# Performance work log

Measured on AMD Instinct MI355X. Metric: run time of the kernel, lower is better.

## Reference

```python
import jax, jax.numpy as jnp
import numpy as np

N_NODES = 100000


def gcn_conv(x, src, dst, W, b):
    # torch_geometric GCNConv: add self-loops, sym-normalize, linear, aggregate
    n = x.shape[0]
    deg = jax.ops.segment_sum(jnp.ones_like(src, dtype=x.dtype), dst, num_segments=n)
    dinv = jnp.where(deg > 0, jax.lax.rsqrt(deg), 0.0)
    norm = dinv[src] * dinv[dst]                      # [E]
    h = x @ W                                         # [N, out]
    msg = h[src] * norm[:, None]                      # [E, out] gather
    out = jax.ops.segment_sum(msg, dst, num_segments=n)  # scatter-add
    return out + b


def add_self_loops(edge_index, n):
    loop = jnp.arange(n, dtype=edge_index.dtype)
    src = jnp.concatenate([edge_index[0], loop])
    dst = jnp.concatenate([edge_index[1], loop])
    return src, dst


def setup_inputs() -> dict:
    key = jax.random.key(0)
    k1, k2, k3, k4 = jax.random.split(key, 4)
    F_in, F_mid = 64, 32
    x = jax.random.normal(k1, (N_NODES, F_in), dtype=jnp.float32)
    edge_index = jax.random.randint(k2, (2, 1200000), 0, N_NODES, dtype=jnp.int64)
    W1 = jax.random.normal(k3, (F_in, F_mid), dtype=jnp.float32) * (1.0 / np.sqrt(F_in))
    b1 = jnp.zeros((F_mid,), dtype=jnp.float32)
    W2 = jax.random.normal(k4, (F_mid, F_in), dtype=jnp.float32) * (1.0 / np.sqrt(F_mid))
    b2 = jnp.zeros((F_in,), dtype=jnp.float32)
    return {"x": x, "edge_index": edge_index, "W1": W1, "b1": b1, "W2": W2, "b2": b2}


def reference(x, edge_index, W1, b1, W2, b2):
    src, dst = add_self_loops(edge_index, x.shape[0])
    h = jax.nn.relu(gcn_conv(x, src, dst, W1, b1))
    # F.dropout in eval mode is identity (module not in training)
    out = gcn_conv(h, src, dst, W2, b2)
    return out
```

## Files before the change

kernel.cpp:

```cpp
#include <hip/hip_runtime.h>


#define CAP 32
#define OVF_MAX 65536
#define SH_BITS 8
#define SH 256
#define BCAP 3584
#define EPB 4096
#define EPT 16

__device__ __forceinline__ unsigned bf16rn(float f) {
    unsigned u = __float_as_uint(f);
    return (u + 0x7fffu + ((u >> 16) & 1u)) >> 16;
}
__device__ __forceinline__ unsigned pack2(float f0, float f1) {
    return (bf16rn(f1) << 16) | bf16rn(f0);
}
__device__ __forceinline__ void acc2(float4& a, uint2 v) {
    a.x += __uint_as_float(v.x << 16);
    a.y += __uint_as_float(v.x & 0xffff0000u);
    a.z += __uint_as_float(v.y << 16);
    a.w += __uint_as_float(v.y & 0xffff0000u);
}

__global__ void init_kernel(int* __restrict__ bcur, int* __restrict__ ovfcnt,
                            unsigned int* __restrict__ g1rowN,
                            unsigned int* __restrict__ q1rowN, int B) {
    int i = blockIdx.x * blockDim.x + threadIdx.x;
    if (i < B) bcur[i] = i * BCAP;
    if (i == 0) *ovfcnt = 0;
    if (i < 16) { g1rowN[i] = 0u; q1rowN[i] = 0u; }
}

__global__ __launch_bounds__(256) void bin_kernel(const int* __restrict__ src,
                                                  const int* __restrict__ dst,
                                                  int* __restrict__ bcur,
                                                  unsigned int* __restrict__ ebuf,
                                                  int* __restrict__ ovfcnt,
                                                  int* __restrict__ ovf, int E, int B) {
    __shared__ int h[512];
    __shared__ int gp[512];
    __shared__ int lr[512];
    for (int b = threadIdx.x; b < B; b += 256) { h[b] = 0; lr[b] = 0; }
    __syncthreads();
    int base = blockIdx.x * EPB;
    int s[EPT], d[EPT], bk[EPT];
#pragma unroll
    for (int k = 0; k < EPT; ++k) {
        int e = base + k * 256 + threadIdx.x;
        bool ok = e < E;
        s[k]  = ok ? src[e] : 0;
        d[k]  = ok ? dst[e] : 0;
        bk[k] = ok ? (d[k] >> SH_BITS) : -1;
        if (ok) atomicAdd(&h[bk[k]], 1);
    }
    __syncthreads();
    for (int b = threadIdx.x; b < B; b += 256)
        if (h[b]) gp[b] = atomicAdd(&bcur[b], h[b]);
    __syncthreads();
#pragma unroll
    for (int k = 0; k < EPT; ++k) {
        if (bk[k] >= 0) {
            int r = atomicAdd(&lr[bk[k]], 1);
            int pos = gp[bk[k]] + r;
            if (pos < (bk[k] + 1) * BCAP)
                ebuf[pos] = ((unsigned)(d[k] & (SH - 1)) << 24) | (unsigned)s[k];
            else { int o = atomicAdd(ovfcnt, 1); if (o < OVF_MAX) { ovf[2 * o] = s[k]; ovf[2 * o + 1] = d[k]; } }
        }
    }
}

__global__ __launch_bounds__(256) void fillb_kernel(const unsigned int* __restrict__ ebuf,
                                                    const int* __restrict__ bcur,
                                                    int* __restrict__ adj,
                                                    float* __restrict__ dinv,
                                                    int* __restrict__ ovfcnt,
                                                    int* __restrict__ ovf, int N) {
    __shared__ int lcnt[SH];
    __shared__ int ladj[SH * CAP];
    int b = blockIdx.x;
    for (int i = threadIdx.x; i < SH; i += 256) lcnt[i] = 0;
    for (int i = threadIdx.x; i < SH * CAP; i += 256) ladj[i] = N;
    __syncthreads();
    int beg = b * BCAP;
    int tot = bcur[b] - beg;
    int m = tot < BCAP ? tot : BCAP;
    for (int i = threadIdx.x; i < m; i += 256) {
        unsigned p = ebuf[beg + i];
        int ld = (int)(p >> 24), sidx = (int)(p & 0xFFFFFF);
        int q = atomicAdd(&lcnt[ld], 1);
        if (q < CAP) ladj[ld * CAP + q] = sidx;
        else { int o = atomicAdd(ovfcnt, 1); if (o < OVF_MAX) { ovf[2 * o] = sidx; ovf[2 * o + 1] = (b << SH_BITS) + ld; } }
    }
    __syncthreads();
    int nb0 = b << SH_BITS;
    const int4* l4 = (const int4*)ladj;
    int4* a4 = (int4*)(adj + (size_t)nb0 * CAP);
    for (int i = threadIdx.x; i < SH * CAP / 4; i += 256) {
        int nd = nb0 + (i * 4) / CAP;
        if (nd < N) a4[i] = l4[i];
    }
    for (int i = threadIdx.x; i < SH; i += 256) {
        int nd = nb0 + i;
        if (nd < N) dinv[nd] = rsqrtf((float)lcnt[i] + 1.0f);
    }
}

__global__ __launch_bounds__(256) void gemm1_kernel(const float* __restrict__ x,
                                                    const float* __restrict__ W1,
                                                    const float* __restrict__ dinv,
                                                    unsigned int* __restrict__ g1, int N) {
    __shared__ float Ws[64 * 32];
    __shared__ float xs[16][64];
    int tid = threadIdx.x;
    const float4* W4 = (const float4*)W1;
    float4* Ws4 = (float4*)Ws;
    for (int i = tid; i < 512; i += 256) Ws4[i] = W4[i];
    int nb = blockIdx.x * 16;
    {
        int ln = tid >> 4, k4 = (tid & 15) * 4;
        int n = nb + ln;
        float4 v = make_float4(0.f, 0.f, 0.f, 0.f);
        if (n < N) v = *(const float4*)(x + (size_t)n * 64 + k4);
        *(float4*)(&xs[ln][k4]) = v;
    }
    __syncthreads();
    int ln = tid >> 4, j = tid & 15;
    int n = nb + ln;
    if (n < N) {
        float s0 = 0.f, s1 = 0.f;
#pragma unroll
        for (int k = 0; k < 64; ++k) {
            float xv = xs[ln][k];
            s0 += xv * Ws[k * 32 + 2 * j];
            s1 += xv * Ws[k * 32 + 2 * j + 1];
        }
        float dv = dinv[n];
        g1[(size_t)n * 16 + j] = pack2(dv * s0, dv * s1);
    }
}

__device__ __forceinline__ float4 gather_row4(const int4* __restrict__ adj4,
                                              const int* __restrict__ ovfcnt,
                                              const int* __restrict__ ovf,
                                              const uint2* __restrict__ g2,
                                              int n, int l, int N) {
    int4 idx = adj4[(size_t)n * 8 + l];
    float4 a = make_float4(0.f, 0.f, 0.f, 0.f);
    uint2 self = g2[(size_t)n * 8 + l];
    {
        int s0  = __shfl(idx.x, 0, 8), s1  = __shfl(idx.y, 0, 8);
        int s2  = __shfl(idx.z, 0, 8), s3  = __shfl(idx.w, 0, 8);
        int s4  = __shfl(idx.x, 1, 8), s5  = __shfl(idx.y, 1, 8);
        int s6  = __shfl(idx.z, 1, 8), s7  = __shfl(idx.w, 1, 8);
        int s8  = __shfl(idx.x, 2, 8), s9  = __shfl(idx.y, 2, 8);
        int s10 = __shfl(idx.z, 2, 8), s11 = __shfl(idx.w, 2, 8);
        int s12 = __shfl(idx.x, 3, 8), s13 = __shfl(idx.y, 3, 8);
        int s14 = __shfl(idx.z, 3, 8), s15 = __shfl(idx.w, 3, 8);
        uint2 v0  = g2[(size_t)s0  * 8 + l], v1  = g2[(size_t)s1  * 8 + l];
        uint2 v2  = g2[(size_t)s2  * 8 + l], v3  = g2[(size_t)s3  * 8 + l];
        uint2 v4  = g2[(size_t)s4  * 8 + l], v5  = g2[(size_t)s5  * 8 + l];
        uint2 v6  = g2[(size_t)s6  * 8 + l], v7  = g2[(size_t)s7  * 8 + l];
        uint2 v8  = g2[(size_t)s8  * 8 + l], v9  = g2[(size_t)s9  * 8 + l];
        uint2 v10 = g2[(size_t)s10 * 8 + l], v11 = g2[(size_t)s11 * 8 + l];
        uint2 v12 = g2[(size_t)s12 * 8 + l], v13 = g2[(size_t)s13 * 8 + l];
        uint2 v14 = g2[(size_t)s14 * 8 + l], v15 = g2[(size_t)s15 * 8 + l];
        acc2(a, self);
        acc2(a, v0);  acc2(a, v1);  acc2(a, v2);  acc2(a, v3);
        acc2(a, v4);  acc2(a, v5);  acc2(a, v6);  acc2(a, v7);
        acc2(a, v8);  acc2(a, v9);  acc2(a, v10); acc2(a, v11);
        acc2(a, v12); acc2(a, v13); acc2(a, v14); acc2(a, v15);
    }
    if (__shfl(idx.x, 4, 8) != N) {
        int s0  = __shfl(idx.x, 4, 8), s1  = __shfl(idx.y, 4, 8);
        int s2  = __shfl(idx.z, 4, 8), s3  = __shfl(idx.w, 4, 8);
        int s4  = __shfl(idx.x, 5, 8), s5  = __shfl(idx.y, 5, 8);
        int s6  = __shfl(idx.z, 5, 8), s7  = __shfl(idx.w, 5, 8);
        int s8  = __shfl(idx.x, 6, 8), s9  = __shfl(idx.y, 6, 8);
        int s10 = __shfl(idx.z, 6, 8), s11 = __shfl(idx.w, 6, 8);
        int s12 = __shfl(idx.x, 7, 8), s13 = __shfl(idx.y, 7, 8);
        int s14 = __shfl(idx.z, 7, 8), s15 = __shfl(idx.w, 7, 8);
        uint2 v0  = g2[(size_t)s0  * 8 + l], v1  = g2[(size_t)s1  * 8 + l];
        uint2 v2  = g2[(size_t)s2  * 8 + l], v3  = g2[(size_t)s3  * 8 + l];
        uint2 v4  = g2[(size_t)s4  * 8 + l], v5  = g2[(size_t)s5  * 8 + l];
        uint2 v6  = g2[(size_t)s6  * 8 + l], v7  = g2[(size_t)s7  * 8 + l];
        uint2 v8  = g2[(size_t)s8  * 8 + l], v9  = g2[(size_t)s9  * 8 + l];
        uint2 v10 = g2[(size_t)s10 * 8 + l], v11 = g2[(size_t)s11 * 8 + l];
        uint2 v12 = g2[(size_t)s12 * 8 + l], v13 = g2[(size_t)s13 * 8 + l];
        uint2 v14 = g2[(size_t)s14 * 8 + l], v15 = g2[(size_t)s15 * 8 + l];
        acc2(a, v0);  acc2(a, v1);  acc2(a, v2);  acc2(a, v3);
        acc2(a, v4);  acc2(a, v5);  acc2(a, v6);  acc2(a, v7);
        acc2(a, v8);  acc2(a, v9);  acc2(a, v10); acc2(a, v11);
        acc2(a, v12); acc2(a, v13); acc2(a, v14); acc2(a, v15);
    }
    int c = *ovfcnt; if (c > OVF_MAX) c = OVF_MAX;
    for (int i = 0; i < c; ++i) {
        if (ovf[2 * i + 1] == n) acc2(a, g2[(size_t)ovf[2 * i] * 8 + l]);
    }
    return a;
}

__global__ void gather_q_kernel(const int4* __restrict__ adj4,
                                const int* __restrict__ ovfcnt, const int* __restrict__ ovf,
                                const uint2* __restrict__ g2, const float* __restrict__ dinv,
                                const float* __restrict__ b1, uint2* __restrict__ q2, int N) {
    int tid = blockIdx.x * blockDim.x + threadIdx.x;
    int n = tid >> 3, l = tid & 7;
    if (n < N) {
        float4 a = gather_row4(adj4, ovfcnt, ovf, g2, n, l, N);
        float dv = dinv[n];
        float4 bb = ((const float4*)b1)[l];
        float vx = dv * a.x + bb.x, vy = dv * a.y + bb.y;
        float vz = dv * a.z + bb.z, vw = dv * a.w + bb.w;
        vx = vx > 0.f ? vx : 0.f; vy = vy > 0.f ? vy : 0.f;
        vz = vz > 0.f ? vz : 0.f; vw = vw > 0.f ? vw : 0.f;
        q2[(size_t)n * 8 + l] = make_uint2(pack2(dv * vx, dv * vy), pack2(dv * vz, dv * vw));
    }
}

__global__ __launch_bounds__(256) void gather_out_kernel(
        const int4* __restrict__ adj4,
        const int* __restrict__ ovfcnt, const int* __restrict__ ovf,
        const uint2* __restrict__ q2, const float* __restrict__ dinv,
        const float* __restrict__ W2, const float* __restrict__ b2,
        float* __restrict__ out, int N) {
    __shared__ float Ws[32 * 64];
    __shared__ float sAgg[32][36];
    int tid = threadIdx.x;
    const float4* W4 = (const float4*)W2;
    float4* Ws4 = (float4*)Ws;
    for (int i = tid; i < 512; i += 256) Ws4[i] = W4[i];
    int nb = blockIdx.x * 32;
    int o = tid >> 3, l = tid & 7;
    int n = nb + o;
    if (n < N) *(float4*)(&sAgg[o][l * 4]) = gather_row4(adj4, ovfcnt, ovf, q2, n, l, N);
    __syncthreads();
    int ln = tid >> 6, j = tid & 63;
#pragma unroll
    for (int nn = 0; nn < 8; ++nn) {
        int ol = nn * 4 + ln;
        int node = nb + ol;
        if (node < N) {
            float s = 0.f;
#pragma unroll
            for (int k = 0; k < 32; ++k) s += sAgg[ol][k] * Ws[k * 64 + j];
            out[(size_t)node * 64 + j] = dinv[node] * s + b2[j];
        }
    }
}

extern "C" void kernel_launch(void* const* d_in, const int* in_sizes, int n_in,
                              void* d_out, int out_size, void* d_ws, size_t ws_size,
                              hipStream_t stream) {
    const float* x  = (const float*)d_in[0];
    const int*   ei = (const int*)d_in[1];
    const float* W1 = (const float*)d_in[2];
    const float* b1 = (const float*)d_in[3];
    const float* W2 = (const float*)d_in[4];
    const float* b2 = (const float*)d_in[5];
    float* out = (float*)d_out;

    int N = in_sizes[0] / 64;
    int E = in_sizes[1] / 2;
    const int* src = ei;
    const int* dst = ei + (size_t)E;
    int B = (N + SH - 1) >> SH_BITS;

    size_t NP = (size_t)N + 1;
    float* dinv   = (float*)d_ws;
    unsigned int* g1 = (unsigned int*)(dinv + N);
    unsigned int* q1 = g1 + 16 * NP;
    unsigned int* ebuf = q1;
    int*   adj    = (int*)(q1 + 16 * NP);
    int*   bcur   = adj + (size_t)CAP * N;
    int*   ovfcnt = bcur + 512;
    int*   ovf    = ovfcnt + 4;

    init_kernel<<<(B + 255) / 256, 256, 0, stream>>>(bcur, ovfcnt,
                                                     g1 + 16 * (size_t)N, q1 + 16 * (size_t)N, B);
    bin_kernel<<<(E + EPB - 1) / EPB, 256, 0, stream>>>(src, dst, bcur, ebuf, ovfcnt, ovf, E, B);
    fillb_kernel<<<B, 256, 0, stream>>>(ebuf, bcur, adj, dinv, ovfcnt, ovf, N);

    gemm1_kernel<<<(N + 15) / 16, 256, 0, stream>>>(x, W1, dinv, g1, N);

    long long tq = (long long)N * 8;
    gather_q_kernel<<<(int)((tq + 255) / 256), 256, 0, stream>>>(
        (const int4*)adj, ovfcnt, ovf, (const uint2*)g1, dinv, b1, (uint2*)q1, N);
    gather_out_kernel<<<(N + 31) / 32, 256, 0, stream>>>(
        (const int4*)adj, ovfcnt, ovf, (const uint2*)q1, dinv, W2, b2, out, N);
}
```

Before: 178.2 us.

## Skip unused adjacency halves, reuse bin-kernel atomic ranks, add nontemporal output stores

The adjacency list is now read in two 64-byte halves, and the second half is loaded only when the 16th slot of the first half is occupied. fillb writes the second half only for nodes with at least 16 neighbours. bin_kernel keeps the rank returned by the histogram atomic, which removes the second shared-memory counter and its atomics. The final output uses nontemporal stores. The aim is to cut adjacency memory traffic and atomics, at the cost of a dependent second load for high-degree nodes and relying on stale memory never being read.

```diff
diff --git a/kernel.cpp b/kernel.cpp
--- a/kernel.cpp
+++ b/kernel.cpp
@@ -40,19 +40,17 @@
                                                   int* __restrict__ ovf, int E, int B) {
     __shared__ int h[512];
     __shared__ int gp[512];
-    __shared__ int lr[512];
-    for (int b = threadIdx.x; b < B; b += 256) { h[b] = 0; lr[b] = 0; }
+    for (int b = threadIdx.x; b < B; b += 256) h[b] = 0;
     __syncthreads();
     int base = blockIdx.x * EPB;
-    int s[EPT], d[EPT], bk[EPT];
+    int s[EPT], d[EPT], r[EPT];
 #pragma unroll
     for (int k = 0; k < EPT; ++k) {
         int e = base + k * 256 + threadIdx.x;
         bool ok = e < E;
-        s[k]  = ok ? src[e] : 0;
-        d[k]  = ok ? dst[e] : 0;
-        bk[k] = ok ? (d[k] >> SH_BITS) : -1;
-        if (ok) atomicAdd(&h[bk[k]], 1);
+        s[k] = ok ? src[e] : 0;
+        d[k] = ok ? dst[e] : 0;
+        r[k] = ok ? atomicAdd(&h[d[k] >> SH_BITS], 1) : 0;
     }
     __syncthreads();
     for (int b = threadIdx.x; b < B; b += 256)
@@ -60,10 +58,11 @@
     __syncthreads();
 #pragma unroll
     for (int k = 0; k < EPT; ++k) {
-        if (bk[k] >= 0) {
-            int r = atomicAdd(&lr[bk[k]], 1);
-            int pos = gp[bk[k]] + r;
-            if (pos < (bk[k] + 1) * BCAP)
+        int e = base + k * 256 + threadIdx.x;
+        if (e < E) {
+            int bk = d[k] >> SH_BITS;
+            int pos = gp[bk] + r[k];
+            if (pos < (bk + 1) * BCAP)
                 ebuf[pos] = ((unsigned)(d[k] & (SH - 1)) << 24) | (unsigned)s[k];
             else { int o = atomicAdd(ovfcnt, 1); if (o < OVF_MAX) { ovf[2 * o] = s[k]; ovf[2 * o + 1] = d[k]; } }
         }
@@ -97,8 +96,10 @@
     const int4* l4 = (const int4*)ladj;
     int4* a4 = (int4*)(adj + (size_t)nb0 * CAP);
     for (int i = threadIdx.x; i < SH * CAP / 4; i += 256) {
-        int nd = nb0 + (i * 4) / CAP;
-        if (nd < N) a4[i] = l4[i];
+        int row = i >> 3;
+        int nd = nb0 + row;
+        bool second = (i & 4) != 0;
+        if (nd < N && (!second || lcnt[row] >= 16)) a4[i] = l4[i];
     }
     for (int i = threadIdx.x; i < SH; i += 256) {
         int nd = nb0 + i;
@@ -140,23 +141,24 @@
     }
 }
 
-__device__ __forceinline__ float4 gather_row4(const int4* __restrict__ adj4,
+__device__ __forceinline__ float4 gather_row4(const int2* __restrict__ adj2,
                                               const int* __restrict__ ovfcnt,
                                               const int* __restrict__ ovf,
                                               const uint2* __restrict__ g2,
                                               int n, int l, int N) {
-    int4 idx = adj4[(size_t)n * 8 + l];
+    int2 h1 = adj2[(size_t)n * 16 + l];
     float4 a = make_float4(0.f, 0.f, 0.f, 0.f);
     uint2 self = g2[(size_t)n * 8 + l];
+    int s15;
     {
-        int s0  = __shfl(idx.x, 0, 8), s1  = __shfl(idx.y, 0, 8);
-        int s2  = __shfl(idx.z, 0, 8), s3  = __shfl(idx.w, 0, 8);
-        int s4  = __shfl(idx.x, 1, 8), s5  = __shfl(idx.y, 1, 8);
-        int s6  = __shfl(idx.z, 1, 8), s7  = __shfl(idx.w, 1, 8);
-        int s8  = __shfl(idx.x, 2, 8), s9  = __shfl(idx.y, 2, 8);
-        int s10 = __shfl(idx.z, 2, 8), s11 = __shfl(idx.w, 2, 8);
-        int s12 = __shfl(idx.x, 3, 8), s13 = __shfl(idx.y, 3, 8);
-        int s14 = __shfl(idx.z, 3, 8), s15 = __shfl(idx.w, 3, 8);
+        int s0  = __shfl(h1.x, 0, 8), s1  = __shfl(h1.y, 0, 8);
+        int s2  = __shfl(h1.x, 1, 8), s3  = __shfl(h1.y, 1, 8);
+        int s4  = __shfl(h1.x, 2, 8), s5  = __shfl(h1.y, 2, 8);
+        int s6  = __shfl(h1.x, 3, 8), s7  = __shfl(h1.y, 3, 8);
+        int s8  = __shfl(h1.x, 4, 8), s9  = __shfl(h1.y, 4, 8);
+        int s10 = __shfl(h1.x, 5, 8), s11 = __shfl(h1.y, 5, 8);
+        int s12 = __shfl(h1.x, 6, 8), s13 = __shfl(h1.y, 6, 8);
+        int s14 = __shfl(h1.x, 7, 8); s15 = __shfl(h1.y, 7, 8);
         uint2 v0  = g2[(size_t)s0  * 8 + l], v1  = g2[(size_t)s1  * 8 + l];
         uint2 v2  = g2[(size_t)s2  * 8 + l], v3  = g2[(size_t)s3  * 8 + l];
         uint2 v4  = g2[(size_t)s4  * 8 + l], v5  = g2[(size_t)s5  * 8 + l];
@@ -171,15 +173,16 @@
         acc2(a, v8);  acc2(a, v9);  acc2(a, v10); acc2(a, v11);
         acc2(a, v12); acc2(a, v13); acc2(a, v14); acc2(a, v15);
     }
-    if (__shfl(idx.x, 4, 8) != N) {
-        int s0  = __shfl(idx.x, 4, 8), s1  = __shfl(idx.y, 4, 8);
-        int s2  = __shfl(idx.z, 4, 8), s3  = __shfl(idx.w, 4, 8);
-        int s4  = __shfl(idx.x, 5, 8), s5  = __shfl(idx.y, 5, 8);
-        int s6  = __shfl(idx.z, 5, 8), s7  = __shfl(idx.w, 5, 8);
-        int s8  = __shfl(idx.x, 6, 8), s9  = __shfl(idx.y, 6, 8);
-        int s10 = __shfl(idx.z, 6, 8), s11 = __shfl(idx.w, 6, 8);
-        int s12 = __shfl(idx.x, 7, 8), s13 = __shfl(idx.y, 7, 8);
-        int s14 = __shfl(idx.z, 7, 8), s15 = __shfl(idx.w, 7, 8);
+    if (s15 != N) {
+        int2 h2 = adj2[(size_t)n * 16 + 8 + l];
+        int s0  = __shfl(h2.x, 0, 8), s1  = __shfl(h2.y, 0, 8);
+        int s2  = __shfl(h2.x, 1, 8), s3  = __shfl(h2.y, 1, 8);
+        int s4  = __shfl(h2.x, 2, 8), s5  = __shfl(h2.y, 2, 8);
+        int s6  = __shfl(h2.x, 3, 8), s7  = __shfl(h2.y, 3, 8);
+        int s8  = __shfl(h2.x, 4, 8), s9  = __shfl(h2.y, 4, 8);
+        int s10 = __shfl(h2.x, 5, 8), s11 = __shfl(h2.y, 5, 8);
+        int s12 = __shfl(h2.x, 6, 8), s13 = __shfl(h2.y, 6, 8);
+        int s14 = __shfl(h2.x, 7, 8), sl15 = __shfl(h2.y, 7, 8);
         uint2 v0  = g2[(size_t)s0  * 8 + l], v1  = g2[(size_t)s1  * 8 + l];
         uint2 v2  = g2[(size_t)s2  * 8 + l], v3  = g2[(size_t)s3  * 8 + l];
         uint2 v4  = g2[(size_t)s4  * 8 + l], v5  = g2[(size_t)s5  * 8 + l];
@@ -187,7 +190,7 @@
         uint2 v8  = g2[(size_t)s8  * 8 + l], v9  = g2[(size_t)s9  * 8 + l];
         uint2 v10 = g2[(size_t)s10 * 8 + l], v11 = g2[(size_t)s11 * 8 + l];
         uint2 v12 = g2[(size_t)s12 * 8 + l], v13 = g2[(size_t)s13 * 8 + l];
-        uint2 v14 = g2[(size_t)s14 * 8 + l], v15 = g2[(size_t)s15 * 8 + l];
+        uint2 v14 = g2[(size_t)s14 * 8 + l], v15 = g2[(size_t)sl15 * 8 + l];
         acc2(a, v0);  acc2(a, v1);  acc2(a, v2);  acc2(a, v3);
         acc2(a, v4);  acc2(a, v5);  acc2(a, v6);  acc2(a, v7);
         acc2(a, v8);  acc2(a, v9);  acc2(a, v10); acc2(a, v11);
@@ -200,14 +203,14 @@
     return a;
 }
 
-__global__ void gather_q_kernel(const int4* __restrict__ adj4,
+__global__ void gather_q_kernel(const int2* __restrict__ adj2,
                                 const int* __restrict__ ovfcnt, const int* __restrict__ ovf,
                                 const uint2* __restrict__ g2, const float* __restrict__ dinv,
                                 const float* __restrict__ b1, uint2* __restrict__ q2, int N) {
     int tid = blockIdx.x * blockDim.x + threadIdx.x;
     int n = tid >> 3, l = tid & 7;
     if (n < N) {
-        float4 a = gather_row4(adj4, ovfcnt, ovf, g2, n, l, N);
+        float4 a = gather_row4(adj2, ovfcnt, ovf, g2, n, l, N);
         float dv = dinv[n];
         float4 bb = ((const float4*)b1)[l];
         float vx = dv * a.x + bb.x, vy = dv * a.y + bb.y;
@@ -219,7 +222,7 @@
 }
 
 __global__ __launch_bounds__(256) void gather_out_kernel(
-        const int4* __restrict__ adj4,
+        const int2* __restrict__ adj2,
         const int* __restrict__ ovfcnt, const int* __restrict__ ovf,
         const uint2* __restrict__ q2, const float* __restrict__ dinv,
         const float* __restrict__ W2, const float* __restrict__ b2,
@@ -233,7 +236,7 @@
     int nb = blockIdx.x * 32;
     int o = tid >> 3, l = tid & 7;
     int n = nb + o;
-    if (n < N) *(float4*)(&sAgg[o][l * 4]) = gather_row4(adj4, ovfcnt, ovf, q2, n, l, N);
+    if (n < N) *(float4*)(&sAgg[o][l * 4]) = gather_row4(adj2, ovfcnt, ovf, q2, n, l, N);
     __syncthreads();
     int ln = tid >> 6, j = tid & 63;
 #pragma unroll
@@ -244,7 +247,7 @@
             float s = 0.f;
 #pragma unroll
             for (int k = 0; k < 32; ++k) s += sAgg[ol][k] * Ws[k * 64 + j];
-            out[(size_t)node * 64 + j] = dinv[node] * s + b2[j];
+            __builtin_nontemporal_store(dinv[node] * s + b2[j], &out[(size_t)node * 64 + j]);
         }
     }
 }
@@ -285,7 +288,7 @@
 
     long long tq = (long long)N * 8;
     gather_q_kernel<<<(int)((tq + 255) / 256), 256, 0, stream>>>(
-        (const int4*)adj, ovfcnt, ovf, (const uint2*)g1, dinv, b1, (uint2*)q1, N);
+        (const int2*)adj, ovfcnt, ovf, (const uint2*)g1, dinv, b1, (uint2*)q1, N);
     gather_out_kernel<<<(N + 31) / 32, 256, 0, stream>>>(
-        (const int4*)adj, ovfcnt, ovf, (const uint2*)q1, dinv, W2, b2, out, N);
-}
+        (const int2*)adj, ovfcnt, ovf, (const uint2*)q1, dinv, W2, b2, out, N);
+}
```

Result: no change. 179.9 us (median of 2 runs) (+1.0%).
